# Optimization experiments

Hardware: AMD Instinct MI355X
Metric: run time of the kernel (lower is better)

The kernel has to match this reference:

```python
import jax, jax.numpy as jnp
import numpy as np

B, L, D = 2, 4096, 768
H, HD = 12, 64
EPS = 1e-6


def setup_inputs() -> dict:
    key = jax.random.key(0)
    ks = jax.random.split(key, 5)
    x = jax.random.normal(ks[0], (B, L, D), dtype=jnp.float32)
    # realistic rope tables
    inv_freq = 1.0 / (10000.0 ** (np.arange(0, HD, 2, dtype=np.float32) / HD))
    t = np.arange(L, dtype=np.float32)
    freqs = np.outer(t, inv_freq)  # (L, HD/2)
    emb = np.concatenate([freqs, freqs], axis=-1)  # (L, HD)
    rope_cos = jnp.asarray(np.cos(emb))
    rope_sin = jnp.asarray(np.sin(emb))
    Wqkv = jax.random.normal(ks[1], (3 * D, D), dtype=jnp.float32) * (1.0 / np.sqrt(D))
    Wout = jax.random.normal(ks[2], (D, D), dtype=jnp.float32) * (1.0 / np.sqrt(D))
    q_norm_w = jnp.ones((HD,), dtype=jnp.float32)
    k_norm_w = jnp.ones((HD,), dtype=jnp.float32)
    return {"x": x, "rope_cos": rope_cos, "rope_sin": rope_sin,
            "Wqkv": Wqkv, "Wout": Wout,
            "q_norm_w": q_norm_w, "k_norm_w": k_norm_w}


def _rms_norm(x, w):
    # x: (..., HD); computed in float32 like the torch module
    norm = jax.lax.rsqrt(jnp.mean(jnp.square(x.astype(jnp.float32)), axis=-1, keepdims=True) + EPS)
    return (x.astype(jnp.float32) * norm).astype(x.dtype) * w


def _rotate_half(x):
    x1, x2 = jnp.split(x, 2, axis=-1)
    return jnp.concatenate([-x2, x1], axis=-1)


def reference(x, rope_cos, rope_sin, Wqkv, Wout, q_norm_w, k_norm_w):
    b, l, d = x.shape
    # fused QKV projection (Linear with no bias): x @ Wqkv.T
    qkv = jnp.einsum('bld,ed->ble', x, Wqkv).reshape(b, l, 3, H, HD)
    q, k, v = qkv[:, :, 0], qkv[:, :, 1], qkv[:, :, 2]  # (B, L, H, HD)
    q = jnp.transpose(q, (0, 2, 1, 3))  # (B, H, L, HD)
    k = jnp.transpose(k, (0, 2, 1, 3))
    v = jnp.transpose(v, (0, 2, 1, 3))
    # per-head RMSNorm on q and k
    q = _rms_norm(q, q_norm_w)
    k = _rms_norm(k, k_norm_w)
    # RoPE: cos/sin (L, HD) broadcast over (B, H)
    cos = rope_cos[None, None, :, :]
    sin = rope_sin[None, None, :, :]
    q = q * cos + _rotate_half(q) * sin
    k = k * cos + _rotate_half(k) * sin
    # scaled dot product attention (no mask)
    scale = 1.0 / jnp.sqrt(jnp.asarray(HD, dtype=q.dtype))
    scores = jnp.einsum('bhqd,bhkd->bhqk', q, k) * scale  # (B, H, L, L)
    attn = jax.nn.softmax(scores, axis=-1)
    out = jnp.einsum('bhqk,bhkd->bhqd', attn, v)  # (B, H, L, HD)
    out = jnp.transpose(out, (0, 2, 1, 3)).reshape(b, l, d)
    return jnp.einsum('bld,ed->ble', out, Wout)
```

## Files before the change

kernel.cpp:

```cpp
#include <hip/hip_runtime.h>
#include <hip/hip_bf16.h>

typedef float f32x4 __attribute__((ext_vector_type(4)));
typedef short bf16x8 __attribute__((ext_vector_type(8)));
typedef unsigned short ushort8_t __attribute__((ext_vector_type(8)));

#define L_SEQ 4096
#define DMODEL 768
#define NHEAD 12
#define HDIM 64

__device__ __forceinline__ unsigned short f2bf(float f) {
    __hip_bfloat16 h = __float2bfloat16(f);
    return *reinterpret_cast<unsigned short*>(&h);
}

__device__ __forceinline__ float bf2f(unsigned short u) {
    return __uint_as_float((unsigned)u << 16);
}

__device__ __forceinline__ unsigned pack2bf(float a, float b) {
    return (unsigned)f2bf(a) | ((unsigned)f2bf(b) << 16);
}

__device__ __forceinline__ void gload16(const void* g, void* l) {
    __builtin_amdgcn_global_load_lds(
        (const __attribute__((address_space(1))) unsigned int*)g,
        (__attribute__((address_space(3))) unsigned int*)l, 16, 0, 0);
}

__global__ __launch_bounds__(256) void cvt_f32_bf16(
    const float* __restrict__ in, unsigned short* __restrict__ out, int n)
{
    int i = (blockIdx.x * 256 + threadIdx.x) * 4;
    if (i + 3 < n) {
        float4 v = *reinterpret_cast<const float4*>(in + i);
        ushort4 o;
        o.x = f2bf(v.x); o.y = f2bf(v.y); o.z = f2bf(v.z); o.w = f2bf(v.w);
        *reinterpret_cast<ushort4*>(out + i) = o;
    }
}

#define BM 128
#define BN 128
#define BKK 64

template <bool BF16OUT>
__global__ __launch_bounds__(256) void gemm_bf16_nt(
    const unsigned short* __restrict__ A, const unsigned short* __restrict__ Bt,
    void* __restrict__ Cv, int M, int N, int K)
{
    __shared__ unsigned short As[BM][BKK];
    __shared__ unsigned short Bs[BN][BKK];
    const int tid  = threadIdx.x;
    const int lane = tid & 63;
    const int wid  = tid >> 6;
    const int r = lane & 15, g = lane >> 4;
    const int wr = wid >> 1, wc = wid & 1;
    const int m0 = blockIdx.y * BM;
    const int n0 = blockIdx.x * BN;

    f32x4 acc[4][4];
    for (int i = 0; i < 4; ++i)
        for (int j = 0; j < 4; ++j)
            acc[i][j] = (f32x4){0.f, 0.f, 0.f, 0.f};

    for (int kt = 0; kt < K; kt += BKK) {
        __syncthreads();
        for (int p = 0; p < 4; ++p) {
            int idx = wid * 64 + p * 256 + lane;
            int row = idx >> 3;
            int ch  = (idx & 7) * 8;
            gload16(&A[(size_t)(m0 + row) * K + kt + ch],
                    (char*)As + (size_t)(wid * 64 + p * 256) * 16);
            gload16(&Bt[(size_t)(n0 + row) * K + kt + ch],
                    (char*)Bs + (size_t)(wid * 64 + p * 256) * 16);
        }
        __syncthreads();
        for (int k0 = 0; k0 < BKK; k0 += 32) {
            bf16x8 a[4], b[4];
            for (int i = 0; i < 4; ++i)
                a[i] = *reinterpret_cast<const bf16x8*>(&As[wr * 64 + i * 16 + r][k0 + 8 * g]);
            for (int j = 0; j < 4; ++j)
                b[j] = *reinterpret_cast<const bf16x8*>(&Bs[wc * 64 + j * 16 + r][k0 + 8 * g]);
            for (int i = 0; i < 4; ++i)
                for (int j = 0; j < 4; ++j)
                    acc[i][j] = __builtin_amdgcn_mfma_f32_16x16x32_bf16(a[i], b[j], acc[i][j], 0, 0, 0);
        }
    }
    for (int i = 0; i < 4; ++i)
        for (int j = 0; j < 4; ++j)
            for (int t = 0; t < 4; ++t) {
                int row = m0 + wr * 64 + i * 16 + 4 * g + t;
                int col = n0 + wc * 64 + j * 16 + r;
                if (BF16OUT)
                    ((unsigned short*)Cv)[(size_t)row * N + col] = f2bf(acc[i][j][t]);
                else
                    ((float*)Cv)[(size_t)row * N + col] = acc[i][j][t];
            }
}

__global__ __launch_bounds__(256) void normrope(
    const unsigned short* __restrict__ qkv, const float* __restrict__ cosb,
    const float* __restrict__ sinb, const float* __restrict__ qw,
    const float* __restrict__ kw,
    unsigned short* __restrict__ Qb, unsigned short* __restrict__ Kb,
    unsigned short* __restrict__ Vt)
{
    __shared__ unsigned short vt[64][66];
    int blk = blockIdx.x;
    int lt = blk & 63;
    int bh = blk >> 6;
    int b = bh / NHEAD, h = bh % NHEAD;
    int wid = threadIdx.x >> 6, lane = threadIdx.x & 63;
    float qwv = qw[lane], kwv = kw[lane];
    float sgn = (lane < 32) ? -1.f : 1.f;

    for (int i = 0; i < 16; ++i) {
        int ll = wid * 16 + i;
        int l = lt * 64 + ll;
        size_t rowb = ((size_t)(b * L_SEQ + l)) * (3 * DMODEL) + h * HDIM + lane;
        float qv = bf2f(qkv[rowb]);
        float kv = bf2f(qkv[rowb + DMODEL]);
        unsigned short vv = qkv[rowb + 2 * DMODEL];
        float sq = qv * qv, sk = kv * kv;
        for (int off = 32; off; off >>= 1) {
            sq += __shfl_xor(sq, off);
            sk += __shfl_xor(sk, off);
        }
        float qn = qv * rsqrtf(sq * (1.f / 64.f) + 1e-6f) * qwv;
        float kn = kv * rsqrtf(sk * (1.f / 64.f) + 1e-6f) * kwv;
        float c = cosb[l * HDIM + lane], s = sinb[l * HDIM + lane];
        float qo = __shfl_xor(qn, 32), ko = __shfl_xor(kn, 32);
        float qr = qn * c + sgn * qo * s;
        float kr = kn * c + sgn * ko * s;
        qr *= 0.125f * 1.44269504f;
        size_t o = ((size_t)bh * L_SEQ + l) * HDIM + lane;
        Qb[o] = f2bf(qr);
        Kb[o] = f2bf(kr);
        vt[ll][lane] = vv;
    }
    __syncthreads();
    for (int i = 0; i < 16; ++i) {
        int d = wid * 16 + i;
        Vt[((size_t)bh * HDIM + d) * L_SEQ + lt * 64 + lane] = vt[lane][d];
    }
}

__global__ __launch_bounds__(256, 3) void flashattn(
    const unsigned short* __restrict__ Qb, const unsigned short* __restrict__ Kb,
    const unsigned short* __restrict__ Vt, unsigned short* __restrict__ aob)
{
    __shared__ unsigned short Ks[2][64 * 64];
    __shared__ unsigned short Vs[2][64 * 64];
    __shared__ unsigned short Ps[4][32 * 64];

    const int bh = blockIdx.y;
    const int b = bh / NHEAD, h = bh % NHEAD;
    const int tid = threadIdx.x;
    const int wid = tid >> 6, lane = tid & 63;
    const int r = lane & 15, g = lane >> 4;
    const int q0 = blockIdx.x * 128 + wid * 32;
    const int rsw = (r & 7) << 4;

    bf16x8 qf[2][2];
    for (int i = 0; i < 2; ++i) {
        const unsigned short* Qp = Qb + ((size_t)bh * L_SEQ + q0 + i * 16 + r) * HDIM + 8 * g;
        qf[i][0] = *reinterpret_cast<const bf16x8*>(Qp);
        qf[i][1] = *reinterpret_cast<const bf16x8*>(Qp + 32);
    }

    bf16x8 onesf;
    for (int e = 0; e < 8; ++e) onesf[e] = (r == 0) ? (short)0x3F80 : (short)0;

    const unsigned short* Kbase = Kb + (size_t)bh * L_SEQ * HDIM;
    const unsigned short* Vbase = Vt + (size_t)bh * HDIM * L_SEQ;
    char* PsB = (char*)Ps[wid];

    f32x4 o[2][4];
    for (int i = 0; i < 2; ++i)
        for (int j = 0; j < 4; ++j) o[i][j] = (f32x4){0.f, 0.f, 0.f, 0.f};
    f32x4 o_l[2];
    o_l[0] = (f32x4){0.f, 0.f, 0.f, 0.f};
    o_l[1] = (f32x4){0.f, 0.f, 0.f, 0.f};

    auto stage = [&](int buf, int kb) {
        for (int p = 0; p < 2; ++p) {
            int idx = wid * 64 + p * 256 + lane;
            int row = idx >> 3;
            int colb = ((idx & 7) * 16) ^ ((row & 7) << 4);
            gload16(Kbase + (size_t)(kb + row) * HDIM + (colb >> 1),
                    (char*)Ks[buf] + (size_t)(wid * 64 + p * 256) * 16);
            gload16(Vbase + (size_t)row * L_SEQ + kb + (colb >> 1),
                    (char*)Vs[buf] + (size_t)(wid * 64 + p * 256) * 16);
        }
    };

    stage(0, 0);
    __syncthreads();
    int cur = 0;

    for (int kb = 0; kb < L_SEQ; kb += 64) {
        if (kb + 64 < L_SEQ) stage(cur ^ 1, kb + 64);
        char* KsB = (char*)Ks[cur];
        char* VsB = (char*)Vs[cur];

        f32x4 s[2][4];
        for (int i = 0; i < 2; ++i)
            for (int kt = 0; kt < 4; ++kt) s[i][kt] = (f32x4){0.f, 0.f, 0.f, 0.f};
        for (int kt = 0; kt < 4; ++kt) {
            bf16x8 kf0 = *reinterpret_cast<const bf16x8*>(KsB + (kt * 16 + r) * 128 + ((16 * g) ^ rsw));
            bf16x8 kf1 = *reinterpret_cast<const bf16x8*>(KsB + (kt * 16 + r) * 128 + ((64 + 16 * g) ^ rsw));
            for (int i = 0; i < 2; ++i) {
                s[i][kt] = __builtin_amdgcn_mfma_f32_16x16x32_bf16(kf0, qf[i][0], s[i][kt], 0, 0, 0);
                s[i][kt] = __builtin_amdgcn_mfma_f32_16x16x32_bf16(kf1, qf[i][1], s[i][kt], 0, 0, 0);
            }
        }

        for (int i = 0; i < 2; ++i) {
            for (int kt = 0; kt < 4; ++kt) {
                float p0 = __builtin_amdgcn_exp2f(s[i][kt][0]);
                float p1 = __builtin_amdgcn_exp2f(s[i][kt][1]);
                float p2 = __builtin_amdgcn_exp2f(s[i][kt][2]);
                float p3 = __builtin_amdgcn_exp2f(s[i][kt][3]);
                uint2 w2;
                w2.x = pack2bf(p0, p1);
                w2.y = pack2bf(p2, p3);
                int dst = (i * 16 + r) * 128 + ((kt * 32 + 8 * g) ^ rsw);
                *reinterpret_cast<uint2*>(PsB + dst) = w2;
            }
        }

        bf16x8 pa[2][2];
        for (int i = 0; i < 2; ++i) {
            pa[i][0] = *reinterpret_cast<const bf16x8*>(PsB + (i * 16 + r) * 128 + ((16 * g) ^ rsw));
            pa[i][1] = *reinterpret_cast<const bf16x8*>(PsB + (i * 16 + r) * 128 + ((64 + 16 * g) ^ rsw));
        }
        for (int i = 0; i < 2; ++i) {
            o_l[i] = __builtin_amdgcn_mfma_f32_16x16x32_bf16(pa[i][0], onesf, o_l[i], 0, 0, 0);
            o_l[i] = __builtin_amdgcn_mfma_f32_16x16x32_bf16(pa[i][1], onesf, o_l[i], 0, 0, 0);
        }
        for (int j = 0; j < 4; ++j) {
            bf16x8 vf0 = *reinterpret_cast<const bf16x8*>(VsB + (j * 16 + r) * 128 + ((16 * g) ^ rsw));
            bf16x8 vf1 = *reinterpret_cast<const bf16x8*>(VsB + (j * 16 + r) * 128 + ((64 + 16 * g) ^ rsw));
            for (int i = 0; i < 2; ++i) {
                o[i][j] = __builtin_amdgcn_mfma_f32_16x16x32_bf16(pa[i][0], vf0, o[i][j], 0, 0, 0);
                o[i][j] = __builtin_amdgcn_mfma_f32_16x16x32_bf16(pa[i][1], vf1, o[i][j], 0, 0, 0);
            }
        }
        __syncthreads();
        cur ^= 1;
    }

    for (int i = 0; i < 2; ++i) {
        float i0 = 1.f / __shfl(o_l[i][0], 16 * g);
        float i1 = 1.f / __shfl(o_l[i][1], 16 * g);
        float i2 = 1.f / __shfl(o_l[i][2], 16 * g);
        float i3 = 1.f / __shfl(o_l[i][3], 16 * g);
        for (int j = 0; j < 4; ++j) {
            size_t base = ((size_t)(b * L_SEQ + q0 + i * 16 + 4 * g)) * DMODEL + h * HDIM + j * 16 + r;
            aob[base] = f2bf(o[i][j][0] * i0);
            aob[base + DMODEL] = f2bf(o[i][j][1] * i1);
            aob[base + 2 * DMODEL] = f2bf(o[i][j][2] * i2);
            aob[base + 3 * DMODEL] = f2bf(o[i][j][3] * i3);
        }
    }
}

extern "C" void kernel_launch(void* const* d_in, const int* in_sizes, int n_in,
                              void* d_out, int out_size, void* d_ws, size_t ws_size,
                              hipStream_t stream) {
    const float* x        = (const float*)d_in[0];
    const float* rope_cos = (const float*)d_in[1];
    const float* rope_sin = (const float*)d_in[2];
    const float* Wqkv     = (const float*)d_in[3];
    const float* Wout     = (const float*)d_in[4];
    const float* q_norm_w = (const float*)d_in[5];
    const float* k_norm_w = (const float*)d_in[6];
    float* out = (float*)d_out;

    const int BL = 2 * L_SEQ;
    const int nx    = BL * DMODEL;
    const int nwqkv = 3 * DMODEL * DMODEL;
    const int nwout = DMODEL * DMODEL;
    const int nqkv  = BL * 3 * DMODEL;

    char* w = (char*)d_ws;
    unsigned short* xb    = (unsigned short*)w; w += (size_t)nx * 2;
    unsigned short* wqkvb = (unsigned short*)w; w += (size_t)nwqkv * 2;
    unsigned short* woutb = (unsigned short*)w; w += (size_t)nwout * 2;
    unsigned short* Qb    = (unsigned short*)w; w += (size_t)nx * 2;
    unsigned short* Kb    = (unsigned short*)w; w += (size_t)nx * 2;
    unsigned short* Vtb   = (unsigned short*)w; w += (size_t)nx * 2;
    unsigned short* qkvb  = (unsigned short*)w; w += (size_t)nqkv * 2;
    unsigned short* aob = qkvb;

    cvt_f32_bf16<<<nx / 1024, 256, 0, stream>>>(x, xb, nx);
    cvt_f32_bf16<<<nwqkv / 1024, 256, 0, stream>>>(Wqkv, wqkvb, nwqkv);
    cvt_f32_bf16<<<nwout / 1024, 256, 0, stream>>>(Wout, woutb, nwout);

    {
        dim3 grid(3 * DMODEL / BN, BL / BM);
        gemm_bf16_nt<true><<<grid, 256, 0, stream>>>(xb, wqkvb, qkvb, BL, 3 * DMODEL, DMODEL);
    }

    normrope<<<24 * 64, 256, 0, stream>>>(qkvb, rope_cos, rope_sin, q_norm_w, k_norm_w,
                                          Qb, Kb, Vtb);

    {
        dim3 grid(L_SEQ / 128, 24);
        flashattn<<<grid, 256, 0, stream>>>(Qb, Kb, Vtb, aob);
    }

    {
        dim3 grid(DMODEL / BN, BL / BM);
        gemm_bf16_nt<false><<<grid, 256, 0, stream>>>(aob, woutb, out, BL, DMODEL, DMODEL);
    }
}
```

Before: 239.3 us.

## Fuse QK RMSNorm, RoPE and V transpose into QKV GEMM epilogue; add MFMA priority hints

```diff
diff --git a/kernel.cpp b/kernel.cpp
--- a/kernel.cpp
+++ b/kernel.cpp
@@ -9,14 +9,11 @@
 #define DMODEL 768
 #define NHEAD 12
 #define HDIM 64
+#define QSCALE (0.125f * 1.44269504f)
 
 __device__ __forceinline__ unsigned short f2bf(float f) {
     __hip_bfloat16 h = __float2bfloat16(f);
     return *reinterpret_cast<unsigned short*>(&h);
-}
-
-__device__ __forceinline__ float bf2f(unsigned short u) {
-    return __uint_as_float((unsigned)u << 16);
 }
 
 __device__ __forceinline__ unsigned pack2bf(float a, float b) {
@@ -45,10 +42,122 @@
 #define BN 128
 #define BKK 64
 
-template <bool BF16OUT>
+__global__ __launch_bounds__(256) void gemm_qkv_fused(
+    const unsigned short* __restrict__ A, const unsigned short* __restrict__ Bt,
+    const float* __restrict__ cosb, const float* __restrict__ sinb,
+    const float* __restrict__ qw, const float* __restrict__ kw,
+    unsigned short* __restrict__ Qb, unsigned short* __restrict__ Kb,
+    unsigned short* __restrict__ Vt)
+{
+    __shared__ union SM {
+        struct { unsigned short As[BM][BKK]; unsigned short Bs[BN][BKK]; } st;
+        unsigned short ep[4][64][72];
+    } sm;
+
+    const int K = DMODEL, M_ = 2 * L_SEQ;
+    const int tid  = threadIdx.x;
+    const int lane = tid & 63;
+    const int wid  = tid >> 6;
+    const int r = lane & 15, g = lane >> 4;
+    const int wr = wid >> 1, wc = wid & 1;
+    const int m0 = blockIdx.y * BM;
+    const int n0 = blockIdx.x * BN;
+    (void)M_;
+
+    f32x4 acc[4][4];
+    for (int i = 0; i < 4; ++i)
+        for (int j = 0; j < 4; ++j)
+            acc[i][j] = (f32x4){0.f, 0.f, 0.f, 0.f};
+
+    for (int kt = 0; kt < K; kt += BKK) {
+        __syncthreads();
+        for (int p = 0; p < 4; ++p) {
+            int idx = wid * 64 + p * 256 + lane;
+            int row = idx >> 3;
+            int ch  = (idx & 7) * 8;
+            gload16(&A[(size_t)(m0 + row) * K + kt + ch],
+                    (char*)sm.st.As + (size_t)(wid * 64 + p * 256) * 16);
+            gload16(&Bt[(size_t)(n0 + row) * K + kt + ch],
+                    (char*)sm.st.Bs + (size_t)(wid * 64 + p * 256) * 16);
+        }
+        __syncthreads();
+        for (int k0 = 0; k0 < BKK; k0 += 32) {
+            bf16x8 a[4], b[4];
+            for (int i = 0; i < 4; ++i)
+                a[i] = *reinterpret_cast<const bf16x8*>(&sm.st.As[wr * 64 + i * 16 + r][k0 + 8 * g]);
+            for (int j = 0; j < 4; ++j)
+                b[j] = *reinterpret_cast<const bf16x8*>(&sm.st.Bs[wc * 64 + j * 16 + r][k0 + 8 * g]);
+            for (int i = 0; i < 4; ++i)
+                for (int j = 0; j < 4; ++j)
+                    acc[i][j] = __builtin_amdgcn_mfma_f32_16x16x32_bf16(a[i], b[j], acc[i][j], 0, 0, 0);
+        }
+    }
+
+    __syncthreads();
+
+    const int e0  = n0 + wc * 64;
+    const int sec = e0 / DMODEL;
+    const int h   = (e0 % DMODEL) / HDIM;
+    const int row0 = m0 + wr * 64;
+    const int b   = row0 >> 12;
+    const int l0  = row0 & (L_SEQ - 1);
+    unsigned short (*ep)[72] = sm.ep[wid];
+
+    if (sec < 2) {
+        const float* nw = (sec == 0) ? qw : kw;
+        float wv[4];
+        for (int j = 0; j < 4; ++j) wv[j] = nw[j * 16 + r];
+        for (int i = 0; i < 4; ++i) {
+            for (int t = 0; t < 4; ++t) {
+                float ss = acc[i][0][t] * acc[i][0][t] + acc[i][1][t] * acc[i][1][t]
+                         + acc[i][2][t] * acc[i][2][t] + acc[i][3][t] * acc[i][3][t];
+                ss += __shfl_xor(ss, 1);
+                ss += __shfl_xor(ss, 2);
+                ss += __shfl_xor(ss, 4);
+                ss += __shfl_xor(ss, 8);
+                float inv = rsqrtf(ss * (1.f / 64.f) + 1e-6f);
+                int lr = i * 16 + 4 * g + t;
+                int l  = l0 + lr;
+                float qn[4];
+                for (int j = 0; j < 4; ++j) qn[j] = acc[i][j][t] * inv * wv[j];
+                for (int j = 0; j < 4; ++j) {
+                    int d = j * 16 + r;
+                    float c = cosb[l * HDIM + d], s = sinb[l * HDIM + d];
+                    float sgn = (j < 2) ? -1.f : 1.f;
+                    float res = qn[j] * c + sgn * qn[j ^ 2] * s;
+                    if (sec == 0) res *= QSCALE;
+                    ep[lr][d] = f2bf(res);
+                }
+            }
+        }
+        unsigned short* dst = ((sec == 0) ? Qb : Kb)
+            + ((size_t)(b * NHEAD + h) * L_SEQ + l0) * HDIM;
+        for (int it = 0; it < 8; ++it) {
+            int idx = it * 64 + lane;
+            int lr = idx >> 3, ch = (idx & 7) * 8;
+            ushort8_t v = *reinterpret_cast<const ushort8_t*>(&ep[lr][ch]);
+            *reinterpret_cast<ushort8_t*>(&dst[(size_t)lr * HDIM + ch]) = v;
+        }
+    } else {
+        for (int i = 0; i < 4; ++i)
+            for (int t = 0; t < 4; ++t) {
+                int lr = i * 16 + 4 * g + t;
+                for (int j = 0; j < 4; ++j)
+                    ep[j * 16 + r][lr] = f2bf(acc[i][j][t]);
+            }
+        unsigned short* dst = Vt + ((size_t)(b * NHEAD + h) * HDIM) * L_SEQ + l0;
+        for (int it = 0; it < 8; ++it) {
+            int idx = it * 64 + lane;
+            int d = idx >> 3, ch = (idx & 7) * 8;
+            ushort8_t v = *reinterpret_cast<const ushort8_t*>(&ep[d][ch]);
+            *reinterpret_cast<ushort8_t*>(&dst[(size_t)d * L_SEQ + ch]) = v;
+        }
+    }
+}
+
 __global__ __launch_bounds__(256) void gemm_bf16_nt(
     const unsigned short* __restrict__ A, const unsigned short* __restrict__ Bt,
-    void* __restrict__ Cv, int M, int N, int K)
+    float* __restrict__ C, int M, int N, int K)
 {
     __shared__ unsigned short As[BM][BKK];
     __shared__ unsigned short Bs[BN][BKK];
@@ -93,58 +202,8 @@
             for (int t = 0; t < 4; ++t) {
                 int row = m0 + wr * 64 + i * 16 + 4 * g + t;
                 int col = n0 + wc * 64 + j * 16 + r;
-                if (BF16OUT)
-                    ((unsigned short*)Cv)[(size_t)row * N + col] = f2bf(acc[i][j][t]);
-                else
-                    ((float*)Cv)[(size_t)row * N + col] = acc[i][j][t];
-            }
-}
-
-__global__ __launch_bounds__(256) void normrope(
-    const unsigned short* __restrict__ qkv, const float* __restrict__ cosb,
-    const float* __restrict__ sinb, const float* __restrict__ qw,
-    const float* __restrict__ kw,
-    unsigned short* __restrict__ Qb, unsigned short* __restrict__ Kb,
-    unsigned short* __restrict__ Vt)
-{
-    __shared__ unsigned short vt[64][66];
-    int blk = blockIdx.x;
-    int lt = blk & 63;
-    int bh = blk >> 6;
-    int b = bh / NHEAD, h = bh % NHEAD;
-    int wid = threadIdx.x >> 6, lane = threadIdx.x & 63;
-    float qwv = qw[lane], kwv = kw[lane];
-    float sgn = (lane < 32) ? -1.f : 1.f;
-
-    for (int i = 0; i < 16; ++i) {
-        int ll = wid * 16 + i;
-        int l = lt * 64 + ll;
-        size_t rowb = ((size_t)(b * L_SEQ + l)) * (3 * DMODEL) + h * HDIM + lane;
-        float qv = bf2f(qkv[rowb]);
-        float kv = bf2f(qkv[rowb + DMODEL]);
-        unsigned short vv = qkv[rowb + 2 * DMODEL];
-        float sq = qv * qv, sk = kv * kv;
-        for (int off = 32; off; off >>= 1) {
-            sq += __shfl_xor(sq, off);
-            sk += __shfl_xor(sk, off);
-        }
-        float qn = qv * rsqrtf(sq * (1.f / 64.f) + 1e-6f) * qwv;
-        float kn = kv * rsqrtf(sk * (1.f / 64.f) + 1e-6f) * kwv;
-        float c = cosb[l * HDIM + lane], s = sinb[l * HDIM + lane];
-        float qo = __shfl_xor(qn, 32), ko = __shfl_xor(kn, 32);
-        float qr = qn * c + sgn * qo * s;
-        float kr = kn * c + sgn * ko * s;
-        qr *= 0.125f * 1.44269504f;
-        size_t o = ((size_t)bh * L_SEQ + l) * HDIM + lane;
-        Qb[o] = f2bf(qr);
-        Kb[o] = f2bf(kr);
-        vt[ll][lane] = vv;
-    }
-    __syncthreads();
-    for (int i = 0; i < 16; ++i) {
-        int d = wid * 16 + i;
-        Vt[((size_t)bh * HDIM + d) * L_SEQ + lt * 64 + lane] = vt[lane][d];
-    }
+                C[(size_t)row * N + col] = acc[i][j][t];
+            }
 }
 
 __global__ __launch_bounds__(256, 3) void flashattn(
@@ -208,6 +267,7 @@
         f32x4 s[2][4];
         for (int i = 0; i < 2; ++i)
             for (int kt = 0; kt < 4; ++kt) s[i][kt] = (f32x4){0.f, 0.f, 0.f, 0.f};
+        __builtin_amdgcn_s_setprio(1);
         for (int kt = 0; kt < 4; ++kt) {
             bf16x8 kf0 = *reinterpret_cast<const bf16x8*>(KsB + (kt * 16 + r) * 128 + ((16 * g) ^ rsw));
             bf16x8 kf1 = *reinterpret_cast<const bf16x8*>(KsB + (kt * 16 + r) * 128 + ((64 + 16 * g) ^ rsw));
@@ -216,6 +276,7 @@
                 s[i][kt] = __builtin_amdgcn_mfma_f32_16x16x32_bf16(kf1, qf[i][1], s[i][kt], 0, 0, 0);
             }
         }
+        __builtin_amdgcn_s_setprio(0);
 
         for (int i = 0; i < 2; ++i) {
             for (int kt = 0; kt < 4; ++kt) {
@@ -236,6 +297,7 @@
             pa[i][0] = *reinterpret_cast<const bf16x8*>(PsB + (i * 16 + r) * 128 + ((16 * g) ^ rsw));
             pa[i][1] = *reinterpret_cast<const bf16x8*>(PsB + (i * 16 + r) * 128 + ((64 + 16 * g) ^ rsw));
         }
+        __builtin_amdgcn_s_setprio(1);
         for (int i = 0; i < 2; ++i) {
             o_l[i] = __builtin_amdgcn_mfma_f32_16x16x32_bf16(pa[i][0], onesf, o_l[i], 0, 0, 0);
             o_l[i] = __builtin_amdgcn_mfma_f32_16x16x32_bf16(pa[i][1], onesf, o_l[i], 0, 0, 0);
@@ -248,6 +310,7 @@
                 o[i][j] = __builtin_amdgcn_mfma_f32_16x16x32_bf16(pa[i][1], vf1, o[i][j], 0, 0, 0);
             }
         }
+        __builtin_amdgcn_s_setprio(0);
         __syncthreads();
         cur ^= 1;
     }
@@ -283,7 +346,6 @@
     const int nx    = BL * DMODEL;
     const int nwqkv = 3 * DMODEL * DMODEL;
     const int nwout = DMODEL * DMODEL;
-    const int nqkv  = BL * 3 * DMODEL;
 
     char* w = (char*)d_ws;
     unsigned short* xb    = (unsigned short*)w; w += (size_t)nx * 2;
@@ -292,8 +354,7 @@
     unsigned short* Qb    = (unsigned short*)w; w += (size_t)nx * 2;
     unsigned short* Kb    = (unsigned short*)w; w += (size_t)nx * 2;
     unsigned short* Vtb   = (unsigned short*)w; w += (size_t)nx * 2;
-    unsigned short* qkvb  = (unsigned short*)w; w += (size_t)nqkv * 2;
-    unsigned short* aob = qkvb;
+    unsigned short* aob   = (unsigned short*)w; w += (size_t)nx * 2;
 
     cvt_f32_bf16<<<nx / 1024, 256, 0, stream>>>(x, xb, nx);
     cvt_f32_bf16<<<nwqkv / 1024, 256, 0, stream>>>(Wqkv, wqkvb, nwqkv);
@@ -301,11 +362,9 @@
 
     {
         dim3 grid(3 * DMODEL / BN, BL / BM);
-        gemm_bf16_nt<true><<<grid, 256, 0, stream>>>(xb, wqkvb, qkvb, BL, 3 * DMODEL, DMODEL);
-    }
-
-    normrope<<<24 * 64, 256, 0, stream>>>(qkvb, rope_cos, rope_sin, q_norm_w, k_norm_w,
-                                          Qb, Kb, Vtb);
+        gemm_qkv_fused<<<grid, 256, 0, stream>>>(xb, wqkvb, rope_cos, rope_sin,
+                                                 q_norm_w, k_norm_w, Qb, Kb, Vtb);
+    }
 
     {
         dim3 grid(L_SEQ / 128, 24);
@@ -314,6 +373,6 @@
 
     {
         dim3 grid(DMODEL / BN, BL / BM);
-        gemm_bf16_nt<false><<<grid, 256, 0, stream>>>(aob, woutb, out, BL, DMODEL, DMODEL);
-    }
-}
+        gemm_bf16_nt<<<grid, 256, 0, stream>>>(aob, woutb, out, BL, DMODEL, DMODEL);
+    }
+}
```

Result: faster. 222.5 us (-7.0%).
